# Kernel optimization log

Hardware: AMD Instinct MI355X
Metric: run time of the kernel (lower is better)

Reference implementation:

```python
import jax, jax.numpy as jnp
import numpy as np

N_NODES = 10000
N_EDGES = 320000
IN_DIM = 128
HID = 256


def setup_inputs() -> dict:
    key = jax.random.key(0)
    ks = jax.random.split(key, 10)
    s_in = 1.0 / np.sqrt(IN_DIM)
    s_h = 1.0 / np.sqrt(HID)
    return {
        "x": jax.random.normal(ks[0], (N_NODES, IN_DIM), dtype=jnp.float32),
        "edge_index": jax.random.randint(ks[1], (2, N_EDGES), 0, N_NODES, dtype=jnp.int64),
        # feature_projector Linear(IN_DIM -> HID)
        "Wp": jax.random.uniform(ks[2], (IN_DIM, HID), jnp.float32, -s_in, s_in),
        "bp": jax.random.uniform(ks[3], (HID,), jnp.float32, -s_in, s_in),
        # LSTM(input=HID, hidden=HID) params, torch layout [4H, H], gate order i,f,g,o
        "W_ih": jax.random.uniform(ks[4], (4 * HID, HID), jnp.float32, -s_h, s_h),
        "W_hh": jax.random.uniform(ks[5], (4 * HID, HID), jnp.float32, -s_h, s_h),
        "b_ih": jax.random.uniform(ks[6], (4 * HID,), jnp.float32, -s_h, s_h),
        "b_hh": jax.random.uniform(ks[7], (4 * HID,), jnp.float32, -s_h, s_h),
        # EvolveGCN-O initial weight [H, H] (glorot-style)
        "initial_weight": jax.random.normal(ks[8], (HID, HID), dtype=jnp.float32) * np.sqrt(2.0 / (2 * HID)),
        # GCNConv bias
        "b_gcn": jnp.zeros((HID,), dtype=jnp.float32),
    }


def _forward(x, edge_index, Wp, bp, W_ih, W_hh, b_ih, b_hh, initial_weight, b_gcn):
    n = x.shape[0]
    # 1) feature projection
    h = x @ Wp + bp  # [N, H]
    # 2) EvolveGCN-O: one LSTM step on the weight matrix (rows = batch),
    #    with h0 = c0 = initial_weight; evolved hidden state is the GCN weight.
    gates = initial_weight @ W_ih.T + b_ih + initial_weight @ W_hh.T + b_hh  # [H, 4H]
    i_g, f_g, g_g, o_g = jnp.split(gates, 4, axis=-1)
    c = jax.nn.sigmoid(f_g) * initial_weight + jax.nn.sigmoid(i_g) * jnp.tanh(g_g)
    W = jax.nn.sigmoid(o_g) * jnp.tanh(c)  # [H, H]
    # 3) GCN propagation with fixed W: out = D^{-1/2}(A+I)D^{-1/2} (h W) + b
    hw = h @ W  # [N, H]
    self_loop = jnp.arange(n, dtype=edge_index.dtype)
    src = jnp.concatenate([edge_index[0], self_loop])
    dst = jnp.concatenate([edge_index[1], self_loop])
    ones = jnp.ones(src.shape[0], dtype=hw.dtype)
    deg = jax.ops.segment_sum(ones, dst, num_segments=n)  # in-degree incl. self loop
    dinv = jnp.where(deg > 0, jax.lax.rsqrt(deg), 0.0)
    norm = dinv[src] * dinv[dst]  # [E+N]
    out = jax.ops.segment_sum(hw[src] * norm[:, None], dst, num_segments=n)
    return out + b_gcn


def reference(x, edge_index, Wp, bp, W_ih, W_hh, b_ih, b_hh, initial_weight, b_gcn):
    return _forward(x, edge_index, Wp, bp, W_ih, W_hh, b_ih, b_hh, initial_weight, b_gcn)
```

## Files before the change

kernel.cpp:

```cpp
#include <hip/hip_runtime.h>
#include <math.h>

#define N_NODES 10000
#define N_EDGES 320000
#define IN_DIM  128
#define HID     256
#define CAP     128

#define NB_GATES 128
#define NB_FILL  313
#define NB_XCVT  640

typedef __attribute__((ext_vector_type(8))) short frag_ab;
typedef __attribute__((ext_vector_type(4))) float frag_cd;


__device__ __forceinline__ unsigned bf16rne(float f) {
    union { float f; unsigned u; } c; c.f = f;
    return (c.u + 0x7FFFu + ((c.u >> 16) & 1u)) >> 16;
}

__global__ __launch_bounds__(256)
void k_prep(const int* __restrict__ ei, int* __restrict__ cursor,
            int* __restrict__ bucket, const float* __restrict__ iw,
            const float* __restrict__ wih, const float* __restrict__ whh,
            float* __restrict__ G, const float* __restrict__ x,
            unsigned* __restrict__ xb) {
    __shared__ float smem[6144];
    if (blockIdx.x >= NB_GATES + NB_FILL) {
        int tid = (blockIdx.x - NB_GATES - NB_FILL) * 256 + threadIdx.x;
        const float2* x2 = (const float2*)x;
        #pragma unroll
        for (int it = 0; it < 4; ++it) {
            int idx = tid + it * (NB_XCVT * 256);
            if (idx < N_NODES * 64) {
                float2 v = x2[idx];
                xb[idx] = bf16rne(v.x) | (bf16rne(v.y) << 16);
            }
        }
        return;
    }
    if (blockIdx.x >= NB_GATES) {
        int e = ((blockIdx.x - NB_GATES) * 256 + threadIdx.x) * 4;
        if (e + 3 < N_EDGES) {
            int4 s4 = *(const int4*)&ei[e];
            int4 d4 = *(const int4*)&ei[N_EDGES + e];
            int p0 = atomicAdd(&cursor[d4.x], 1);
            if (p0 < CAP) bucket[d4.x * CAP + p0] = s4.x;
            int p1 = atomicAdd(&cursor[d4.y], 1);
            if (p1 < CAP) bucket[d4.y * CAP + p1] = s4.y;
            int p2 = atomicAdd(&cursor[d4.z], 1);
            if (p2 < CAP) bucket[d4.z * CAP + p2] = s4.z;
            int p3 = atomicAdd(&cursor[d4.w], 1);
            if (p3 < CAP) bucket[d4.w * CAP + p3] = s4.w;
        } else {
            for (int q = e; q < N_EDGES; ++q) {
                int s = ei[q];
                int d = ei[N_EDGES + q];
                int pos = atomicAdd(&cursor[d], 1);
                if (pos < CAP) bucket[d * CAP + pos] = s;
            }
        }
        return;
    }
    int bid = blockIdx.x;
    int m0 = (bid & 7) * 32, n0 = (bid >> 3) * 64;
    float (*aT)[32] = (float(*)[32])smem;
    float (*bS)[64] = (float(*)[64])(smem + 2048);
    int t = threadIdx.x;
    int tm = t & 15, tn = t >> 4;
    float acc[2][4] = {};
    for (int kt = 0; kt < 4; ++kt) {
        int k0 = kt * 64;
        {
            int row = t >> 3;
            #pragma unroll
            for (int r = 0; r < 2; ++r) {
                int kq = 2 * (t & 7) + r;
                float4 av = *(const float4*)&iw[(m0 + row) * HID + k0 + 4 * kq];
                aT[4 * kq + 0][row] = av.x; aT[4 * kq + 1][row] = av.y;
                aT[4 * kq + 2][row] = av.z; aT[4 * kq + 3][row] = av.w;
            }
        }
        {
            int row = t >> 2;
            #pragma unroll
            for (int r = 0; r < 4; ++r) {
                int kq = 4 * (t & 3) + r;
                float4 b1 = *(const float4*)&wih[(n0 + row) * HID + k0 + 4 * kq];
                float4 b2 = *(const float4*)&whh[(n0 + row) * HID + k0 + 4 * kq];
                bS[4 * kq + 0][row] = b1.x + b2.x; bS[4 * kq + 1][row] = b1.y + b2.y;
                bS[4 * kq + 2][row] = b1.z + b2.z; bS[4 * kq + 3][row] = b1.w + b2.w;
            }
        }
        __syncthreads();
        #pragma unroll 8
        for (int kk = 0; kk < 64; ++kk) {
            float2 a2 = *(const float2*)&aT[kk][2 * tm];
            float4 b4 = *(const float4*)&bS[kk][4 * tn];
            float a[2] = {a2.x, a2.y};
            float b[4] = {b4.x, b4.y, b4.z, b4.w};
            #pragma unroll
            for (int i = 0; i < 2; ++i)
                #pragma unroll
                for (int j = 0; j < 4; ++j)
                    acc[i][j] = fmaf(a[i], b[j], acc[i][j]);
        }
        __syncthreads();
    }
    #pragma unroll
    for (int i = 0; i < 2; ++i) {
        float4 o = make_float4(acc[i][0], acc[i][1], acc[i][2], acc[i][3]);
        *(float4*)&G[(m0 + 2 * tm + i) * 1024 + n0 + 4 * tn] = o;
    }
}

__device__ __forceinline__ float sig_f(float x)  { return 1.f / (1.f + __expf(-x)); }
__device__ __forceinline__ float tanh_f(float x) { return 1.f - 2.f / (1.f + __expf(2.f * x)); }

__global__ __launch_bounds__(256)
void k_wev_dinv(const float* __restrict__ G, const float* __restrict__ iw,
                const float* __restrict__ b_ih, const float* __restrict__ b_hh,
                float* __restrict__ Wev, const int* __restrict__ cursor,
                float* __restrict__ dinv) {
    if (blockIdx.x >= 256) {
        int v = (blockIdx.x - 256) * 256 + threadIdx.x;
        if (v < N_NODES) dinv[v] = rsqrtf((float)(cursor[v] + 1));
        return;
    }
    int r = blockIdx.x;
    int j = threadIdx.x;
    float gi = G[r * 1024 + 0   + j] + b_ih[0   + j] + b_hh[0   + j];
    float gf = G[r * 1024 + 256 + j] + b_ih[256 + j] + b_hh[256 + j];
    float gg = G[r * 1024 + 512 + j] + b_ih[512 + j] + b_hh[512 + j];
    float go = G[r * 1024 + 768 + j] + b_ih[768 + j] + b_hh[768 + j];
    float c  = sig_f(gf) * iw[r * HID + j] + sig_f(gi) * tanh_f(gg);
    Wev[r * HID + j] = sig_f(go) * tanh_f(c);
}

__global__ __launch_bounds__(256)
void k_wc_agg(const unsigned* __restrict__ xb, const int* __restrict__ bucket,
              const int* __restrict__ cursor, const float* __restrict__ dinv,
              unsigned* __restrict__ yb, float* __restrict__ rs,
              const float* __restrict__ Wp, const float* __restrict__ bp,
              const float* __restrict__ Wev, unsigned* __restrict__ wct,
              float* __restrict__ bc) {
    __shared__ float arow[HID];
    if (blockIdx.x < 129) {
        int a = blockIdx.x;
        int j = threadIdx.x;
        const float* srcRow = (a < IN_DIM) ? &Wp[a * HID] : bp;
        arow[j] = srcRow[j];
        __syncthreads();
        float acc = 0.f;
        #pragma unroll 4
        for (int k = 0; k < HID; ++k)
            acc = fmaf(arow[k], Wev[k * HID + j], acc);
        if (a < IN_DIM)
            ((unsigned short*)wct)[j * IN_DIM + a] = (unsigned short)bf16rne(acc);
        else
            bc[j] = acc;
        return;
    }
    int wv   = threadIdx.x >> 6;
    int lane = threadIdx.x & 63;
    int v = (blockIdx.x - 129) * 4 + wv;
    int cntv = cursor[v];
    float dv = dinv[v];
    int cnt = cntv > CAP ? CAP : cntv;
    unsigned self = xb[v * 64 + lane];
    union { unsigned u; float f; } c0, c1;
    c0.u = self << 16; c1.u = self & 0xFFFF0000u;
    float acc0 = dv * c0.f, acc1 = dv * c1.f;
    float wsum = dv;
    const int4* bkt4 = (const int4*)&bucket[v * CAP];
    int j = 0;
    for (; j + 4 <= cnt; j += 4) {
        int4 s = bkt4[j >> 2];
        float w0 = dinv[s.x], w1 = dinv[s.y], w2 = dinv[s.z], w3 = dinv[s.w];
        unsigned r0 = xb[s.x * 64 + lane];
        unsigned r1 = xb[s.y * 64 + lane];
        unsigned r2 = xb[s.z * 64 + lane];
        unsigned r3 = xb[s.w * 64 + lane];
        union { unsigned u; float f; } a0, a1;
        a0.u = r0 << 16; a1.u = r0 & 0xFFFF0000u;
        acc0 = fmaf(w0, a0.f, acc0); acc1 = fmaf(w0, a1.f, acc1);
        a0.u = r1 << 16; a1.u = r1 & 0xFFFF0000u;
        acc0 = fmaf(w1, a0.f, acc0); acc1 = fmaf(w1, a1.f, acc1);
        a0.u = r2 << 16; a1.u = r2 & 0xFFFF0000u;
        acc0 = fmaf(w2, a0.f, acc0); acc1 = fmaf(w2, a1.f, acc1);
        a0.u = r3 << 16; a1.u = r3 & 0xFFFF0000u;
        acc0 = fmaf(w3, a0.f, acc0); acc1 = fmaf(w3, a1.f, acc1);
        wsum += w0 + w1 + w2 + w3;
    }
    for (; j < cnt; ++j) {
        int s = ((const int*)bkt4)[j];
        float w = dinv[s];
        unsigned r = xb[s * 64 + lane];
        union { unsigned u; float f; } a0, a1;
        a0.u = r << 16; a1.u = r & 0xFFFF0000u;
        acc0 = fmaf(w, a0.f, acc0); acc1 = fmaf(w, a1.f, acc1);
        wsum += w;
    }
    yb[v * 64 + lane] = bf16rne(dv * acc0) | (bf16rne(dv * acc1) << 16);
    if (lane == 0) rs[v] = dv * wsum;
}

__global__ __launch_bounds__(256)
void k_out(const unsigned* __restrict__ yb, const unsigned* __restrict__ wct,
           const float* __restrict__ bc, const float* __restrict__ rs,
           const float* __restrict__ b_gcn, float* __restrict__ out) {
    int m0 = blockIdx.x * 16;
    int w = threadIdx.x >> 6, lane = threadIdx.x & 63;
    int q = lane >> 4, ln = lane & 15;
    const int4* yb4  = (const int4*)yb;
    const int4* wct4 = (const int4*)wct;
    union { int4 v; frag_ab f; } a[4];
    #pragma unroll
    for (int kc = 0; kc < 4; ++kc)
        a[kc].v = yb4[(m0 + ln) * 16 + kc * 4 + q];
    float rsv[4];
    #pragma unroll
    for (int r = 0; r < 4; ++r) rsv[r] = rs[m0 + q * 4 + r];
    #pragma unroll
    for (int i = 0; i < 4; ++i) {
        int n0 = (w + 4 * i) * 16;
        union { int4 v; frag_ab f; } b[4];
        #pragma unroll
        for (int kc = 0; kc < 4; ++kc)
            b[kc].v = wct4[(n0 + ln) * 16 + kc * 4 + q];
        frag_cd acc = {0.f, 0.f, 0.f, 0.f};
        #pragma unroll
        for (int kc = 0; kc < 4; ++kc)
            acc = __builtin_amdgcn_mfma_f32_16x16x32_bf16(a[kc].f, b[kc].f, acc, 0, 0, 0);
        int n = n0 + ln;
        float bcv = bc[n], bgv = b_gcn[n];
        #pragma unroll
        for (int r = 0; r < 4; ++r) {
            int m = m0 + q * 4 + r;
            out[m * HID + n] = acc[r] + rsv[r] * bcv + bgv;
        }
    }
}

extern "C" void kernel_launch(void* const* d_in, const int* in_sizes, int n_in,
                              void* d_out, int out_size, void* d_ws, size_t ws_size,
                              hipStream_t stream) {
    const float* x     = (const float*)d_in[0];
    const int*   ei    = (const int*)d_in[1];
    const float* Wp    = (const float*)d_in[2];
    const float* bp    = (const float*)d_in[3];
    const float* W_ih  = (const float*)d_in[4];
    const float* W_hh  = (const float*)d_in[5];
    const float* b_ih  = (const float*)d_in[6];
    const float* b_hh  = (const float*)d_in[7];
    const float* iw    = (const float*)d_in[8];
    const float* b_gcn = (const float*)d_in[9];
    float* out = (float*)d_out;

    char* ws = (char*)d_ws;
    unsigned* yb     = (unsigned*)(ws + 0);
    float*    G      = (float*)   (ws + 2560000);
    float*    Wev    = (float*)   (ws + 3608576);
    unsigned* wct    = (unsigned*)(ws + 3870720);
    float*    bc     = (float*)   (ws + 3936256);
    float*    rs     = (float*)   (ws + 3937280);
    unsigned* xb     = (unsigned*)(ws + 3977280);
    int*      cursor = (int*)     (ws + 6537280);
    float*    dinv   = (float*)   (ws + 6577280);
    int*      bucket = (int*)     (ws + 6617280);

    hipMemsetAsync(cursor, 0, N_NODES * sizeof(int), stream);

    k_prep<<<NB_GATES + NB_FILL + NB_XCVT, 256, 0, stream>>>(
        ei, cursor, bucket, iw, W_ih, W_hh, G, x, xb);
    k_wev_dinv<<<256 + 40, 256, 0, stream>>>(G, iw, b_ih, b_hh, Wev, cursor, dinv);
    k_wc_agg<<<129 + 2500, 256, 0, stream>>>(xb, bucket, cursor, dinv, yb, rs, Wp, bp, Wev, wct, bc);
    k_out<<<625, 256, 0, stream>>>(yb, wct, bc, rs, b_gcn, out);
}
```

Baseline: 131.1 us.

## Fuse all stages into one cooperative persistent kernel with grid syncs

Replaces the four separate kernel launches with a single cooperative kernel of 512 blocks that separates the phases with grid-wide syncs. The work is also re-split: the gate GEMM runs alongside x conversion, the edge bucketing runs alongside the LSTM elementwise step, and the Wp·Wev product is batched eight rows per block. The dinv array is dropped and recomputed inline from cursor with rsqrt. The goal is to remove launch gaps and tail effects between kernels, at the cost of grid-sync overhead and fewer blocks to hide latency in the gather-heavy aggregation.

After: 495.2 us. +277.8%, slower.

```diff
diff --git a/kernel.cpp b/kernel.cpp
--- a/kernel.cpp
+++ b/kernel.cpp
@@ -1,15 +1,15 @@
 #include <hip/hip_runtime.h>
+#include <hip/hip_cooperative_groups.h>
 #include <math.h>
+
+namespace cg = cooperative_groups;
 
 #define N_NODES 10000
 #define N_EDGES 320000
 #define IN_DIM  128
 #define HID     256
 #define CAP     128
-
-#define NB_GATES 128
-#define NB_FILL  313
-#define NB_XCVT  640
+#define NBLK    512
 
 typedef __attribute__((ext_vector_type(8))) short frag_ab;
 typedef __attribute__((ext_vector_type(4))) float frag_cd;
@@ -19,32 +19,99 @@
     union { float f; unsigned u; } c; c.f = f;
     return (c.u + 0x7FFFu + ((c.u >> 16) & 1u)) >> 16;
 }
-
-__global__ __launch_bounds__(256)
-void k_prep(const int* __restrict__ ei, int* __restrict__ cursor,
-            int* __restrict__ bucket, const float* __restrict__ iw,
-            const float* __restrict__ wih, const float* __restrict__ whh,
-            float* __restrict__ G, const float* __restrict__ x,
-            unsigned* __restrict__ xb) {
+__device__ __forceinline__ float sig_f(float x)  { return 1.f / (1.f + __expf(-x)); }
+__device__ __forceinline__ float tanh_f(float x) { return 1.f - 2.f / (1.f + __expf(2.f * x)); }
+
+__global__ __launch_bounds__(256, 2)
+void k_fused(const float* __restrict__ x, const int* __restrict__ ei,
+             const float* __restrict__ Wp, const float* __restrict__ bp,
+             const float* __restrict__ wih, const float* __restrict__ whh,
+             const float* __restrict__ b_ih, const float* __restrict__ b_hh,
+             const float* __restrict__ iw, const float* __restrict__ b_gcn,
+             float* __restrict__ out,
+             unsigned* __restrict__ yb, float* __restrict__ G,
+             float* __restrict__ Wev, unsigned* __restrict__ wct,
+             float* __restrict__ bc, float* __restrict__ rs,
+             unsigned* __restrict__ xb, int* __restrict__ cursor,
+             int* __restrict__ bucket) {
     __shared__ float smem[6144];
-    if (blockIdx.x >= NB_GATES + NB_FILL) {
-        int tid = (blockIdx.x - NB_GATES - NB_FILL) * 256 + threadIdx.x;
+    cg::grid_group grid = cg::this_grid();
+    const int bid = blockIdx.x;
+    const int t = threadIdx.x;
+
+    if (bid >= 384) {
+        int gb = bid - 384;
+        int m0 = (gb & 7) * 32, n0 = (gb >> 3) * 64;
+        float (*aT)[32] = (float(*)[32])smem;
+        float (*bS)[64] = (float(*)[64])(smem + 2048);
+        int tm = t & 15, tn = t >> 4;
+        float acc[2][4] = {};
+        for (int kt = 0; kt < 4; ++kt) {
+            int k0 = kt * 64;
+            {
+                int row = t >> 3;
+                #pragma unroll
+                for (int r = 0; r < 2; ++r) {
+                    int kq = 2 * (t & 7) + r;
+                    float4 av = *(const float4*)&iw[(m0 + row) * HID + k0 + 4 * kq];
+                    aT[4 * kq + 0][row] = av.x; aT[4 * kq + 1][row] = av.y;
+                    aT[4 * kq + 2][row] = av.z; aT[4 * kq + 3][row] = av.w;
+                }
+            }
+            {
+                int row = t >> 2;
+                #pragma unroll
+                for (int r = 0; r < 4; ++r) {
+                    int kq = 4 * (t & 3) + r;
+                    float4 b1 = *(const float4*)&wih[(n0 + row) * HID + k0 + 4 * kq];
+                    float4 b2 = *(const float4*)&whh[(n0 + row) * HID + k0 + 4 * kq];
+                    bS[4 * kq + 0][row] = b1.x + b2.x; bS[4 * kq + 1][row] = b1.y + b2.y;
+                    bS[4 * kq + 2][row] = b1.z + b2.z; bS[4 * kq + 3][row] = b1.w + b2.w;
+                }
+            }
+            __syncthreads();
+            #pragma unroll 8
+            for (int kk = 0; kk < 64; ++kk) {
+                float2 a2 = *(const float2*)&aT[kk][2 * tm];
+                float4 b4 = *(const float4*)&bS[kk][4 * tn];
+                float a[2] = {a2.x, a2.y};
+                float b[4] = {b4.x, b4.y, b4.z, b4.w};
+                #pragma unroll
+                for (int i = 0; i < 2; ++i)
+                    #pragma unroll
+                    for (int j = 0; j < 4; ++j)
+                        acc[i][j] = fmaf(a[i], b[j], acc[i][j]);
+            }
+            __syncthreads();
+        }
+        #pragma unroll
+        for (int i = 0; i < 2; ++i) {
+            float4 o = make_float4(acc[i][0], acc[i][1], acc[i][2], acc[i][3]);
+            *(float4*)&G[(m0 + 2 * tm + i) * 1024 + n0 + 4 * tn] = o;
+        }
+    } else {
         const float2* x2 = (const float2*)x;
-        #pragma unroll
-        for (int it = 0; it < 4; ++it) {
-            int idx = tid + it * (NB_XCVT * 256);
-            if (idx < N_NODES * 64) {
-                float2 v = x2[idx];
-                xb[idx] = bf16rne(v.x) | (bf16rne(v.y) << 16);
-            }
-        }
-        return;
-    }
-    if (blockIdx.x >= NB_GATES) {
-        int e = ((blockIdx.x - NB_GATES) * 256 + threadIdx.x) * 4;
-        if (e + 3 < N_EDGES) {
-            int4 s4 = *(const int4*)&ei[e];
-            int4 d4 = *(const int4*)&ei[N_EDGES + e];
+        for (int idx = bid * 256 + t; idx < N_NODES * 64; idx += 384 * 256) {
+            float2 v = x2[idx];
+            xb[idx] = bf16rne(v.x) | (bf16rne(v.y) << 16);
+        }
+    }
+    __threadfence();
+    grid.sync();
+
+    if (bid < 256) {
+        int r = bid, j = t;
+        float gi = G[r * 1024 + 0   + j] + b_ih[0   + j] + b_hh[0   + j];
+        float gf = G[r * 1024 + 256 + j] + b_ih[256 + j] + b_hh[256 + j];
+        float gg = G[r * 1024 + 512 + j] + b_ih[512 + j] + b_hh[512 + j];
+        float go = G[r * 1024 + 768 + j] + b_ih[768 + j] + b_hh[768 + j];
+        float c  = sig_f(gf) * iw[r * HID + j] + sig_f(gi) * tanh_f(gg);
+        Wev[r * HID + j] = sig_f(go) * tanh_f(c);
+    } else {
+        int gid = (bid - 256) * 256 + t;
+        for (int u = gid; u < N_EDGES / 4; u += 256 * 256) {
+            int4 s4 = *(const int4*)&ei[u * 4];
+            int4 d4 = *(const int4*)&ei[N_EDGES + u * 4];
             int p0 = atomicAdd(&cursor[d4.x], 1);
             if (p0 < CAP) bucket[d4.x * CAP + p0] = s4.x;
             int p1 = atomicAdd(&cursor[d4.y], 1);
@@ -53,192 +120,124 @@
             if (p2 < CAP) bucket[d4.z * CAP + p2] = s4.z;
             int p3 = atomicAdd(&cursor[d4.w], 1);
             if (p3 < CAP) bucket[d4.w * CAP + p3] = s4.w;
+        }
+    }
+    __threadfence();
+    grid.sync();
+
+    if (bid < 17) {
+        if (bid < 16) {
+            int a0 = bid * 8;
+            float (*ar)[HID] = (float(*)[HID])smem;
+            #pragma unroll
+            for (int r = 0; r < 8; ++r) ar[r][t] = Wp[(a0 + r) * HID + t];
+            __syncthreads();
+            int j = t;
+            float acc[8] = {};
+            #pragma unroll 4
+            for (int k = 0; k < HID; ++k) {
+                float w = Wev[k * HID + j];
+                #pragma unroll
+                for (int r = 0; r < 8; ++r) acc[r] = fmaf(ar[r][k], w, acc[r]);
+            }
+            uint4 pv;
+            pv.x = bf16rne(acc[0]) | (bf16rne(acc[1]) << 16);
+            pv.y = bf16rne(acc[2]) | (bf16rne(acc[3]) << 16);
+            pv.z = bf16rne(acc[4]) | (bf16rne(acc[5]) << 16);
+            pv.w = bf16rne(acc[6]) | (bf16rne(acc[7]) << 16);
+            *(uint4*)((unsigned short*)wct + j * IN_DIM + a0) = pv;
         } else {
-            for (int q = e; q < N_EDGES; ++q) {
-                int s = ei[q];
-                int d = ei[N_EDGES + q];
-                int pos = atomicAdd(&cursor[d], 1);
-                if (pos < CAP) bucket[d * CAP + pos] = s;
-            }
-        }
-        return;
-    }
-    int bid = blockIdx.x;
-    int m0 = (bid & 7) * 32, n0 = (bid >> 3) * 64;
-    float (*aT)[32] = (float(*)[32])smem;
-    float (*bS)[64] = (float(*)[64])(smem + 2048);
-    int t = threadIdx.x;
-    int tm = t & 15, tn = t >> 4;
-    float acc[2][4] = {};
-    for (int kt = 0; kt < 4; ++kt) {
-        int k0 = kt * 64;
-        {
-            int row = t >> 3;
-            #pragma unroll
-            for (int r = 0; r < 2; ++r) {
-                int kq = 2 * (t & 7) + r;
-                float4 av = *(const float4*)&iw[(m0 + row) * HID + k0 + 4 * kq];
-                aT[4 * kq + 0][row] = av.x; aT[4 * kq + 1][row] = av.y;
-                aT[4 * kq + 2][row] = av.z; aT[4 * kq + 3][row] = av.w;
-            }
-        }
-        {
-            int row = t >> 2;
-            #pragma unroll
-            for (int r = 0; r < 4; ++r) {
-                int kq = 4 * (t & 3) + r;
-                float4 b1 = *(const float4*)&wih[(n0 + row) * HID + k0 + 4 * kq];
-                float4 b2 = *(const float4*)&whh[(n0 + row) * HID + k0 + 4 * kq];
-                bS[4 * kq + 0][row] = b1.x + b2.x; bS[4 * kq + 1][row] = b1.y + b2.y;
-                bS[4 * kq + 2][row] = b1.z + b2.z; bS[4 * kq + 3][row] = b1.w + b2.w;
-            }
-        }
-        __syncthreads();
-        #pragma unroll 8
-        for (int kk = 0; kk < 64; ++kk) {
-            float2 a2 = *(const float2*)&aT[kk][2 * tm];
-            float4 b4 = *(const float4*)&bS[kk][4 * tn];
-            float a[2] = {a2.x, a2.y};
-            float b[4] = {b4.x, b4.y, b4.z, b4.w};
-            #pragma unroll
-            for (int i = 0; i < 2; ++i)
-                #pragma unroll
-                for (int j = 0; j < 4; ++j)
-                    acc[i][j] = fmaf(a[i], b[j], acc[i][j]);
-        }
-        __syncthreads();
-    }
-    #pragma unroll
-    for (int i = 0; i < 2; ++i) {
-        float4 o = make_float4(acc[i][0], acc[i][1], acc[i][2], acc[i][3]);
-        *(float4*)&G[(m0 + 2 * tm + i) * 1024 + n0 + 4 * tn] = o;
-    }
-}
-
-__device__ __forceinline__ float sig_f(float x)  { return 1.f / (1.f + __expf(-x)); }
-__device__ __forceinline__ float tanh_f(float x) { return 1.f - 2.f / (1.f + __expf(2.f * x)); }
-
-__global__ __launch_bounds__(256)
-void k_wev_dinv(const float* __restrict__ G, const float* __restrict__ iw,
-                const float* __restrict__ b_ih, const float* __restrict__ b_hh,
-                float* __restrict__ Wev, const int* __restrict__ cursor,
-                float* __restrict__ dinv) {
-    if (blockIdx.x >= 256) {
-        int v = (blockIdx.x - 256) * 256 + threadIdx.x;
-        if (v < N_NODES) dinv[v] = rsqrtf((float)(cursor[v] + 1));
-        return;
-    }
-    int r = blockIdx.x;
-    int j = threadIdx.x;
-    float gi = G[r * 1024 + 0   + j] + b_ih[0   + j] + b_hh[0   + j];
-    float gf = G[r * 1024 + 256 + j] + b_ih[256 + j] + b_hh[256 + j];
-    float gg = G[r * 1024 + 512 + j] + b_ih[512 + j] + b_hh[512 + j];
-    float go = G[r * 1024 + 768 + j] + b_ih[768 + j] + b_hh[768 + j];
-    float c  = sig_f(gf) * iw[r * HID + j] + sig_f(gi) * tanh_f(gg);
-    Wev[r * HID + j] = sig_f(go) * tanh_f(c);
-}
-
-__global__ __launch_bounds__(256)
-void k_wc_agg(const unsigned* __restrict__ xb, const int* __restrict__ bucket,
-              const int* __restrict__ cursor, const float* __restrict__ dinv,
-              unsigned* __restrict__ yb, float* __restrict__ rs,
-              const float* __restrict__ Wp, const float* __restrict__ bp,
-              const float* __restrict__ Wev, unsigned* __restrict__ wct,
-              float* __restrict__ bc) {
-    __shared__ float arow[HID];
-    if (blockIdx.x < 129) {
-        int a = blockIdx.x;
-        int j = threadIdx.x;
-        const float* srcRow = (a < IN_DIM) ? &Wp[a * HID] : bp;
-        arow[j] = srcRow[j];
-        __syncthreads();
-        float acc = 0.f;
-        #pragma unroll 4
-        for (int k = 0; k < HID; ++k)
-            acc = fmaf(arow[k], Wev[k * HID + j], acc);
-        if (a < IN_DIM)
-            ((unsigned short*)wct)[j * IN_DIM + a] = (unsigned short)bf16rne(acc);
-        else
-            bc[j] = acc;
-        return;
-    }
-    int wv   = threadIdx.x >> 6;
-    int lane = threadIdx.x & 63;
-    int v = (blockIdx.x - 129) * 4 + wv;
-    int cntv = cursor[v];
-    float dv = dinv[v];
-    int cnt = cntv > CAP ? CAP : cntv;
-    unsigned self = xb[v * 64 + lane];
-    union { unsigned u; float f; } c0, c1;
-    c0.u = self << 16; c1.u = self & 0xFFFF0000u;
-    float acc0 = dv * c0.f, acc1 = dv * c1.f;
-    float wsum = dv;
-    const int4* bkt4 = (const int4*)&bucket[v * CAP];
-    int j = 0;
-    for (; j + 4 <= cnt; j += 4) {
-        int4 s = bkt4[j >> 2];
-        float w0 = dinv[s.x], w1 = dinv[s.y], w2 = dinv[s.z], w3 = dinv[s.w];
-        unsigned r0 = xb[s.x * 64 + lane];
-        unsigned r1 = xb[s.y * 64 + lane];
-        unsigned r2 = xb[s.z * 64 + lane];
-        unsigned r3 = xb[s.w * 64 + lane];
-        union { unsigned u; float f; } a0, a1;
-        a0.u = r0 << 16; a1.u = r0 & 0xFFFF0000u;
-        acc0 = fmaf(w0, a0.f, acc0); acc1 = fmaf(w0, a1.f, acc1);
-        a0.u = r1 << 16; a1.u = r1 & 0xFFFF0000u;
-        acc0 = fmaf(w1, a0.f, acc0); acc1 = fmaf(w1, a1.f, acc1);
-        a0.u = r2 << 16; a1.u = r2 & 0xFFFF0000u;
-        acc0 = fmaf(w2, a0.f, acc0); acc1 = fmaf(w2, a1.f, acc1);
-        a0.u = r3 << 16; a1.u = r3 & 0xFFFF0000u;
-        acc0 = fmaf(w3, a0.f, acc0); acc1 = fmaf(w3, a1.f, acc1);
-        wsum += w0 + w1 + w2 + w3;
-    }
-    for (; j < cnt; ++j) {
-        int s = ((const int*)bkt4)[j];
-        float w = dinv[s];
-        unsigned r = xb[s * 64 + lane];
-        union { unsigned u; float f; } a0, a1;
-        a0.u = r << 16; a1.u = r & 0xFFFF0000u;
-        acc0 = fmaf(w, a0.f, acc0); acc1 = fmaf(w, a1.f, acc1);
-        wsum += w;
-    }
-    yb[v * 64 + lane] = bf16rne(dv * acc0) | (bf16rne(dv * acc1) << 16);
-    if (lane == 0) rs[v] = dv * wsum;
-}
-
-__global__ __launch_bounds__(256)
-void k_out(const unsigned* __restrict__ yb, const unsigned* __restrict__ wct,
-           const float* __restrict__ bc, const float* __restrict__ rs,
-           const float* __restrict__ b_gcn, float* __restrict__ out) {
-    int m0 = blockIdx.x * 16;
-    int w = threadIdx.x >> 6, lane = threadIdx.x & 63;
-    int q = lane >> 4, ln = lane & 15;
-    const int4* yb4  = (const int4*)yb;
-    const int4* wct4 = (const int4*)wct;
-    union { int4 v; frag_ab f; } a[4];
-    #pragma unroll
-    for (int kc = 0; kc < 4; ++kc)
-        a[kc].v = yb4[(m0 + ln) * 16 + kc * 4 + q];
-    float rsv[4];
-    #pragma unroll
-    for (int r = 0; r < 4; ++r) rsv[r] = rs[m0 + q * 4 + r];
-    #pragma unroll
-    for (int i = 0; i < 4; ++i) {
-        int n0 = (w + 4 * i) * 16;
-        union { int4 v; frag_ab f; } b[4];
-        #pragma unroll
-        for (int kc = 0; kc < 4; ++kc)
-            b[kc].v = wct4[(n0 + ln) * 16 + kc * 4 + q];
-        frag_cd acc = {0.f, 0.f, 0.f, 0.f};
-        #pragma unroll
-        for (int kc = 0; kc < 4; ++kc)
-            acc = __builtin_amdgcn_mfma_f32_16x16x32_bf16(a[kc].f, b[kc].f, acc, 0, 0, 0);
-        int n = n0 + ln;
-        float bcv = bc[n], bgv = b_gcn[n];
-        #pragma unroll
-        for (int r = 0; r < 4; ++r) {
-            int m = m0 + q * 4 + r;
-            out[m * HID + n] = acc[r] + rsv[r] * bcv + bgv;
+            smem[t] = bp[t];
+            __syncthreads();
+            float acc = 0.f;
+            #pragma unroll 4
+            for (int k = 0; k < HID; ++k)
+                acc = fmaf(smem[k], Wev[k * HID + t], acc);
+            bc[t] = acc;
+        }
+    } else {
+        int wv = t >> 6, lane = t & 63;
+        for (int v = (bid - 17) * 4 + wv; v < N_NODES; v += 495 * 4) {
+            int cntv = cursor[v];
+            float dv = rsqrtf((float)(cntv + 1));
+            int cnt = cntv > CAP ? CAP : cntv;
+            unsigned self = xb[v * 64 + lane];
+            union { unsigned u; float f; } c0, c1;
+            c0.u = self << 16; c1.u = self & 0xFFFF0000u;
+            float acc0 = dv * c0.f, acc1 = dv * c1.f;
+            float wsum = dv;
+            const int4* bkt4 = (const int4*)&bucket[v * CAP];
+            int j = 0;
+            for (; j + 4 <= cnt; j += 4) {
+                int4 s = bkt4[j >> 2];
+                float w0 = rsqrtf((float)(cursor[s.x] + 1));
+                float w1 = rsqrtf((float)(cursor[s.y] + 1));
+                float w2 = rsqrtf((float)(cursor[s.z] + 1));
+                float w3 = rsqrtf((float)(cursor[s.w] + 1));
+                unsigned r0 = xb[s.x * 64 + lane];
+                unsigned r1 = xb[s.y * 64 + lane];
+                unsigned r2 = xb[s.z * 64 + lane];
+                unsigned r3 = xb[s.w * 64 + lane];
+                union { unsigned u; float f; } a0, a1;
+                a0.u = r0 << 16; a1.u = r0 & 0xFFFF0000u;
+                acc0 = fmaf(w0, a0.f, acc0); acc1 = fmaf(w0, a1.f, acc1);
+                a0.u = r1 << 16; a1.u = r1 & 0xFFFF0000u;
+                acc0 = fmaf(w1, a0.f, acc0); acc1 = fmaf(w1, a1.f, acc1);
+                a0.u = r2 << 16; a1.u = r2 & 0xFFFF0000u;
+                acc0 = fmaf(w2, a0.f, acc0); acc1 = fmaf(w2, a1.f, acc1);
+                a0.u = r3 << 16; a1.u = r3 & 0xFFFF0000u;
+                acc0 = fmaf(w3, a0.f, acc0); acc1 = fmaf(w3, a1.f, acc1);
+                wsum += w0 + w1 + w2 + w3;
+            }
+            for (; j < cnt; ++j) {
+                int s = ((const int*)bkt4)[j];
+                float w = rsqrtf((float)(cursor[s] + 1));
+                unsigned r = xb[s * 64 + lane];
+                union { unsigned u; float f; } a0, a1;
+                a0.u = r << 16; a1.u = r & 0xFFFF0000u;
+                acc0 = fmaf(w, a0.f, acc0); acc1 = fmaf(w, a1.f, acc1);
+                wsum += w;
+            }
+            yb[v * 64 + lane] = bf16rne(dv * acc0) | (bf16rne(dv * acc1) << 16);
+            if (lane == 0) rs[v] = dv * wsum;
+        }
+    }
+    __threadfence();
+    grid.sync();
+
+    {
+        int w = t >> 6, lane = t & 63;
+        int q = lane >> 4, ln = lane & 15;
+        const int4* yb4  = (const int4*)yb;
+        const int4* wct4 = (const int4*)wct;
+        for (int tile = bid; tile < 625; tile += NBLK) {
+            int m0 = tile * 16;
+            union { int4 v; frag_ab f; } a[4];
+            #pragma unroll
+            for (int kc = 0; kc < 4; ++kc)
+                a[kc].v = yb4[(m0 + ln) * 16 + kc * 4 + q];
+            float rsv[4];
+            #pragma unroll
+            for (int r = 0; r < 4; ++r) rsv[r] = rs[m0 + q * 4 + r];
+            #pragma unroll
+            for (int i = 0; i < 4; ++i) {
+                int n0 = (w + 4 * i) * 16;
+                union { int4 v; frag_ab f; } b[4];
+                #pragma unroll
+                for (int kc = 0; kc < 4; ++kc)
+                    b[kc].v = wct4[(n0 + ln) * 16 + kc * 4 + q];
+                frag_cd acc = {0.f, 0.f, 0.f, 0.f};
+                #pragma unroll
+                for (int kc = 0; kc < 4; ++kc)
+                    acc = __builtin_amdgcn_mfma_f32_16x16x32_bf16(a[kc].f, b[kc].f, acc, 0, 0, 0);
+                int n = n0 + ln;
+                float bcv = bc[n], bgv = b_gcn[n];
+                #pragma unroll
+                for (int r = 0; r < 4; ++r) {
+                    int m = m0 + q * 4 + r;
+                    out[m * HID + n] = acc[r] + rsv[r] * bcv + bgv;
+                }
+            }
         }
     }
 }
@@ -267,14 +266,16 @@
     float*    rs     = (float*)   (ws + 3937280);
     unsigned* xb     = (unsigned*)(ws + 3977280);
     int*      cursor = (int*)     (ws + 6537280);
-    float*    dinv   = (float*)   (ws + 6577280);
     int*      bucket = (int*)     (ws + 6617280);
 
     hipMemsetAsync(cursor, 0, N_NODES * sizeof(int), stream);
 
-    k_prep<<<NB_GATES + NB_FILL + NB_XCVT, 256, 0, stream>>>(
-        ei, cursor, bucket, iw, W_ih, W_hh, G, x, xb);
-    k_wev_dinv<<<256 + 40, 256, 0, stream>>>(G, iw, b_ih, b_hh, Wev, cursor, dinv);
-    k_wc_agg<<<129 + 2500, 256, 0, stream>>>(xb, bucket, cursor, dinv, yb, rs, Wp, bp, Wev, wct, bc);
-    k_out<<<625, 256, 0, stream>>>(yb, wct, bc, rs, b_gcn, out);
+    void* args[] = {
+        (void*)&x, (void*)&ei, (void*)&Wp, (void*)&bp, (void*)&W_ih, (void*)&W_hh,
+        (void*)&b_ih, (void*)&b_hh, (void*)&iw, (void*)&b_gcn, (void*)&out,
+        (void*)&yb, (void*)&G, (void*)&Wev, (void*)&wct, (void*)&bc, (void*)&rs,
+        (void*)&xb, (void*)&cursor, (void*)&bucket
+    };
+    hipLaunchCooperativeKernel((const void*)k_fused, dim3(NBLK), dim3(256),
+                               args, 0, stream);
 }
```
